# Kernel tuning notes

Hardware: AMD Instinct MI355X
Metric: run time of the kernel (lower is better)

The kernel has to match this reference:

```python
import jax, jax.numpy as jnp
import numpy as np

EPS = 1e-12  # torch F.normalize default eps
K, C = 64, 128  # num_clusters, dim


def _l2norm(v, axis):
    n = jnp.sqrt(jnp.sum(v * v, axis=axis, keepdims=True))
    return v / jnp.maximum(n, EPS)


def setup_inputs() -> dict:
    key = jax.random.key(0)
    k1, k2, k3, k4 = jax.random.split(key, 4)
    x = jax.random.normal(k1, (32, C, 64, 64), dtype=jnp.float32)
    centroids = jax.random.uniform(k2, (K, C), dtype=jnp.float32)
    # conv weight/bias initialized from centroids like _init_params (alpha=100)
    alpha = 100.0
    conv_w = 2.0 * alpha * centroids                     # [K, C] (1x1 conv)
    conv_b = -alpha * jnp.linalg.norm(centroids, axis=1) # [K]
    return {"x": x, "conv_w": conv_w, "conv_b": conv_b, "centroids": centroids}


def reference(x, conv_w, conv_b, centroids):
    N = x.shape[0]
    # descriptor-wise L2 normalization over channel dim
    x = _l2norm(x, axis=1)
    xf = x.reshape(N, C, -1)  # [N, C, P]
    # 1x1 conv == per-location linear: [N, K, P]
    logits = jnp.einsum('kc,ncp->nkp', conv_w, xf) + conv_b[None, :, None]
    soft_assign = jax.nn.softmax(logits, axis=1)  # softmax over clusters
    # vlad[n,k,c] = sum_p a[n,k,p] * (x[n,c,p] - centroids[k,c])
    # algebraic rewrite avoids the O(N*K*C*P) intermediate (same math)
    vlad = jnp.einsum('nkp,ncp->nkc', soft_assign, xf) \
        - soft_assign.sum(axis=2)[:, :, None] * centroids[None]
    vlad = _l2norm(vlad, axis=2)            # intra-normalization over C
    vlad = vlad.reshape(N, -1)              # [N, K*C]
    vlad = _l2norm(vlad, axis=1)            # global L2 norm
    return vlad
```

## Files before the change

kernel.cpp:

```cpp
#include <hip/hip_runtime.h>

typedef __attribute__((ext_vector_type(2))) float f2;
typedef __attribute__((ext_vector_type(4))) float f4;
typedef __attribute__((ext_vector_type(4))) float f32x4;
typedef __attribute__((ext_vector_type(4))) unsigned u32x4;
typedef __attribute__((ext_vector_type(8))) short bf16x8;

#define NK 64
#define NC 128
#define NP 4096
#define NN 32
#define EPSV 1e-12f

#define PCH 64
#define CPB 4
#define NGRPX (NP / (PCH * CPB))

#define WS_WF_SL 0
#define WS_SS    8192
#define WS_VP    (8192 + 32768)
#define WS_SLAB_TOTAL (WS_VP + NGRPX * NN * NK * NC)

#define FB_VLAD 0
#define FB_S    (NN * NK * NC)
#define FB_G    (FB_S + NN * NK)
#define FB_WF   (FB_G + NN)
#define FB_TOTAL (FB_WF + 8192)

__device__ __forceinline__ unsigned short f2bf(float x) {
  unsigned u = __builtin_bit_cast(unsigned, x);
  u += 0x7fffu + ((u >> 16) & 1u);
  return (unsigned short)(u >> 16);
}
__device__ __forceinline__ float bf2f(unsigned short h) {
  unsigned u = ((unsigned)h) << 16;
  return __builtin_bit_cast(float, u);
}
__device__ __forceinline__ unsigned cvtpk(float a, float b) {
  unsigned r;
  asm volatile("v_cvt_pk_bf16_f32 %0, %1, %2" : "=v"(r) : "v"(a), "v"(b));
  return r;
}
__device__ __forceinline__ float asf(unsigned u) { return __builtin_bit_cast(float, u); }

__device__ __forceinline__ void barrier_lds() {
  asm volatile("s_waitcnt lgkmcnt(0)" ::: "memory");
  __builtin_amdgcn_s_barrier();
  asm volatile("" ::: "memory");
  __builtin_amdgcn_sched_barrier(0);
}

__global__ void nv_zero(float* __restrict__ ws) {
  int i = blockIdx.x * blockDim.x + threadIdx.x;
  int stride = gridDim.x * blockDim.x;
  for (; i < FB_WF; i += stride) ws[i] = 0.0f;
}

__global__ void nv_wfrag(const float* __restrict__ conv_w, unsigned short* __restrict__ wfrag) {
  int idx = blockIdx.x * 256 + threadIdx.x;
  if (idx >= 2048) return;
  int lane = idx & 63, hl = (idx >> 6) & 1, ct = (idx >> 7) & 3, kt = idx >> 9;
  int r = lane & 15, g = lane >> 4;
  const float* src = conv_w + (16 * kt + r) * NC + 32 * ct + 8 * g;
  unsigned short o[8];
#pragma unroll
  for (int j = 0; j < 8; ++j) {
    float v = src[j];
    unsigned short h = f2bf(v);
    o[j] = hl ? f2bf(v - bf2f(h)) : h;
  }
  u32x4 pk;
#pragma unroll
  for (int m = 0; m < 4; ++m) pk[m] = (unsigned)o[2 * m] | ((unsigned)o[2 * m + 1] << 16);
  *reinterpret_cast<u32x4*>(wfrag + (size_t)idx * 8) = pk;
}

template <bool SLAB>
__global__ __launch_bounds__(512, 2)
void nv_main(const float* __restrict__ x, const unsigned short* __restrict__ wfrag,
             const float* __restrict__ conv_b, float* __restrict__ vout,
             float* __restrict__ sout) {
  __shared__ __align__(16) unsigned xhl_t[PCH][132];
  __shared__ __align__(16) unsigned short xh[NC][72];
  __shared__ __align__(16) unsigned short a_lds[NK][72];
  __shared__ __align__(16) unsigned short wf_lds[1024][8];
  __shared__ __align__(16) float mx_buf[2][PCH];
  __shared__ __align__(16) float sum_buf[2][PCH];

  const int tid = threadIdx.x;
  const int lane = tid & 63;
  const int w = tid >> 6;
  const int r = lane & 15;
  const int g = lane >> 4;
  const int n = blockIdx.y;
  const int p0loc = (w & 3) << 4;
  const int kp = w >> 2;
  const int ktg0 = kp << 1;
  const int kw = w & 3;
  const int ph = w >> 2;

  for (int s = tid; s < 1024; s += 512) {
    int gs = ((s >> 6) * 2) * 64 + (s & 63);
    *reinterpret_cast<u32x4*>(&wf_lds[s][0]) =
        *reinterpret_cast<const u32x4*>(wfrag + (size_t)gs * 8);
  }
  bf16x8 wlo_r[2][4];
#pragma unroll
  for (int kt2 = 0; kt2 < 2; ++kt2)
#pragma unroll
    for (int ct = 0; ct < 4; ++ct)
      wlo_r[kt2][ct] = *reinterpret_cast<const bf16x8*>(
          wfrag + ((size_t)(((ktg0 + kt2) * 4 + ct) * 2 + 1) * 64 + lane) * 8);
  float bb[2];
#pragma unroll
  for (int kt2 = 0; kt2 < 2; ++kt2) bb[kt2] = conv_b[16 * (ktg0 + kt2) + r];

  f32x4 vacc[8];
#pragma unroll
  for (int t = 0; t < 8; ++t) vacc[t] = (f32x4){0.f, 0.f, 0.f, 0.f};
  float s_part[2] = {0.f, 0.f};

  const int cst = tid & 127;
  const int pq = tid >> 7;
  const int swst = ((cst >> 3) & 3) << 3;
  const int pbase = blockIdx.x * (CPB * PCH);
  const float* xrow = x + ((size_t)n * NC + cst) * NP + 16 * pq;

  f4 pre[4];
  auto STAGE = [&]() {
#pragma unroll
    for (int q4 = 0; q4 < 4; ++q4) {
      f4 v = pre[q4];
      const int pl = 16 * pq + 4 * q4;
      unsigned h01 = cvtpk(v[0], v[1]);
      unsigned h23 = cvtpk(v[2], v[3]);
      float r0 = v[0] - asf(h01 << 16);
      float r1 = v[1] - asf(h01 & 0xffff0000u);
      float r2 = v[2] - asf(h23 << 16);
      float r3 = v[3] - asf(h23 & 0xffff0000u);
      unsigned l01 = cvtpk(r0, r1);
      unsigned l23 = cvtpk(r2, r3);
      const int pp = pl ^ swst;
      *reinterpret_cast<unsigned*>(&xh[cst][pp]) = h01;
      *reinterpret_cast<unsigned*>(&xh[cst][pp + 2]) = h23;
      xhl_t[pl + 0][cst] = __builtin_amdgcn_perm(h01, l01, 0x05040100u);
      xhl_t[pl + 1][cst] = __builtin_amdgcn_perm(h01, l01, 0x07060302u);
      xhl_t[pl + 2][cst] = __builtin_amdgcn_perm(h23, l23, 0x05040100u);
      xhl_t[pl + 3][cst] = __builtin_amdgcn_perm(h23, l23, 0x07060302u);
    }
  };

#pragma unroll
  for (int q4 = 0; q4 < 4; ++q4)
    pre[q4] = *reinterpret_cast<const f4*>(xrow + pbase + 4 * q4);
  STAGE();
  barrier_lds();

  for (int cc = 0; cc < CPB; ++cc) {
    if (cc + 1 < CPB) {
      const float* xb = xrow + pbase + (cc + 1) * PCH;
#pragma unroll
      for (int q4 = 0; q4 < 4; ++q4)
        pre[q4] = *reinterpret_cast<const f4*>(xb + 4 * q4);
    }
    f32x4 d1 = {0.f, 0.f, 0.f, 0.f}, d2 = {0.f, 0.f, 0.f, 0.f};
    f32x4 lac[2];
    lac[0] = (f32x4){0.f, 0.f, 0.f, 0.f};
    lac[1] = (f32x4){0.f, 0.f, 0.f, 0.f};
    __builtin_amdgcn_s_setprio(1);
#pragma unroll
    for (int ct = 0; ct < 4; ++ct) {
      const unsigned* row = &xhl_t[p0loc + r][32 * ct + 8 * g];
      u32x4 wA = *reinterpret_cast<const u32x4*>(row);
      u32x4 wB = *reinterpret_cast<const u32x4*>(row + 4);
      unsigned wv8[8] = {wA[0], wA[1], wA[2], wA[3], wB[0], wB[1], wB[2], wB[3]};
      u32x4 hh, ll;
#pragma unroll
      for (int m = 0; m < 4; ++m) {
        hh[m] = __builtin_amdgcn_perm(wv8[2 * m + 1], wv8[2 * m], 0x07060302u);
        ll[m] = __builtin_amdgcn_perm(wv8[2 * m + 1], wv8[2 * m], 0x05040100u);
      }
      bf16x8 Ah = __builtin_bit_cast(bf16x8, hh);
      bf16x8 Al = __builtin_bit_cast(bf16x8, ll);
      d1 = __builtin_amdgcn_mfma_f32_16x16x32_bf16(Ah, Ah, d1, 0, 0, 0);
      d2 = __builtin_amdgcn_mfma_f32_16x16x32_bf16(Ah, Al, d2, 0, 0, 0);
#pragma unroll
      for (int kt2 = 0; kt2 < 2; ++kt2) {
        const int kt4ct = (ktg0 + kt2) * 4 + ct;
        bf16x8 whi = *reinterpret_cast<const bf16x8*>(&wf_lds[kt4ct * 64 + lane][0]);
        lac[kt2] = __builtin_amdgcn_mfma_f32_16x16x32_bf16(Ah, whi, lac[kt2], 0, 0, 0);
        lac[kt2] = __builtin_amdgcn_mfma_f32_16x16x32_bf16(Al, whi, lac[kt2], 0, 0, 0);
        lac[kt2] = __builtin_amdgcn_mfma_f32_16x16x32_bf16(Ah, wlo_r[kt2][ct], lac[kt2], 0, 0, 0);
      }
    }
    __builtin_amdgcn_s_setprio(0);
    float nsq = d1[r & 3] + 2.0f * d2[r & 3];
    float ivv[4];
#pragma unroll
    for (int i = 0; i < 4; ++i) {
      float ns = __shfl(nsq, 20 * g + i);
      ivv[i] = 1.0f / fmaxf(sqrtf(ns), EPSV);
    }
    float lt[2][4], e[2][4], mpart[4], sp[4];
#pragma unroll
    for (int kt2 = 0; kt2 < 2; ++kt2)
#pragma unroll
      for (int i = 0; i < 4; ++i) lt[kt2][i] = lac[kt2][i] * ivv[i] + bb[kt2];
#pragma unroll
    for (int i = 0; i < 4; ++i) mpart[i] = fmaxf(lt[0][i], lt[1][i]);
#pragma unroll
    for (int o = 1; o <= 8; o <<= 1)
#pragma unroll
      for (int i = 0; i < 4; ++i) mpart[i] = fmaxf(mpart[i], __shfl_xor(mpart[i], o));
#pragma unroll
    for (int i = 0; i < 4; ++i) sp[i] = 0.f;
#pragma unroll
    for (int kt2 = 0; kt2 < 2; ++kt2)
#pragma unroll
      for (int i = 0; i < 4; ++i) {
        e[kt2][i] = __expf(lt[kt2][i] - mpart[i]);
        sp[i] += e[kt2][i];
      }
#pragma unroll
    for (int o = 1; o <= 8; o <<= 1)
#pragma unroll
      for (int i = 0; i < 4; ++i) sp[i] += __shfl_xor(sp[i], o);
    if (r < 4) mx_buf[kp][p0loc + 4 * g + r] = mpart[r];
    else if (r < 8) sum_buf[kp][p0loc + 4 * g + (r - 4)] = sp[r - 4];
    bf16x8 bx[8];
#pragma unroll
    for (int tcl = 0; tcl < 8; ++tcl) {
      const int c = (tcl << 4) + r;
      const int pblk = ((ph << 2) + g) ^ ((c >> 3) & 3);
      bx[tcl] = *reinterpret_cast<const bf16x8*>(&xh[c][pblk << 3]);
    }
    barrier_lds();
    {
      f4 m0 = *reinterpret_cast<const f4*>(&mx_buf[0][p0loc + 4 * g]);
      f4 m1 = *reinterpret_cast<const f4*>(&mx_buf[1][p0loc + 4 * g]);
      f4 s0 = *reinterpret_cast<const f4*>(&sum_buf[0][p0loc + 4 * g]);
      f4 s1 = *reinterpret_cast<const f4*>(&sum_buf[1][p0loc + 4 * g]);
      float fcorr[4];
#pragma unroll
      for (int i = 0; i < 4; ++i) {
        float m = fmaxf(m0[i], m1[i]);
        float c0 = __expf(m0[i] - m);
        float c1 = __expf(m1[i] - m);
        float tot = s0[i] * c0 + s1[i] * c1;
        fcorr[i] = (kp == 0 ? c0 : c1) / tot;
      }
#pragma unroll
      for (int kt2 = 0; kt2 < 2; ++kt2) {
        float av[4];
#pragma unroll
        for (int i = 0; i < 4; ++i) {
          float a = e[kt2][i] * fcorr[i];
          s_part[kt2] += a;
          av[i] = a * ivv[i];
        }
        unsigned* arow = reinterpret_cast<unsigned*>(&a_lds[16 * (ktg0 + kt2) + r][p0loc + 4 * g]);
        arow[0] = cvtpk(av[0], av[1]);
        arow[1] = cvtpk(av[2], av[3]);
      }
    }
    barrier_lds();
    {
      bf16x8 af = *reinterpret_cast<const bf16x8*>(&a_lds[16 * kw + r][32 * ph + 8 * g]);
      __builtin_amdgcn_s_setprio(1);
#pragma unroll
      for (int tcl = 0; tcl < 8; ++tcl)
        vacc[tcl] = __builtin_amdgcn_mfma_f32_16x16x32_bf16(af, bx[tcl], vacc[tcl], 0, 0, 0);
      __builtin_amdgcn_s_setprio(0);
    }
    if (cc + 1 < CPB) {
      STAGE();
      barrier_lds();
    }
  }

  float* cbuf = reinterpret_cast<float*>(&xhl_t[0][0]);
  float* s_red = cbuf + 8192;
  if (w < 4) {
#pragma unroll
    for (int tcl = 0; tcl < 8; ++tcl)
#pragma unroll
      for (int i = 0; i < 4; ++i)
        cbuf[kw * 2048 + (4 * g + i) * 128 + (tcl << 4) + r] = vacc[tcl][i];
  }
#pragma unroll
  for (int kt2 = 0; kt2 < 2; ++kt2) {
    float v = s_part[kt2];
    v += __shfl_xor(v, 16);
    v += __shfl_xor(v, 32);
    if (g == 0) s_red[(kp * 4 + (w & 3)) * 32 + kt2 * 16 + r] = v;
  }
  barrier_lds();
  if (w >= 4) {
#pragma unroll
    for (int tcl = 0; tcl < 8; ++tcl)
#pragma unroll
      for (int i = 0; i < 4; ++i) {
        const int idx = kw * 2048 + (4 * g + i) * 128 + (tcl << 4) + r;
        float v = vacc[tcl][i] + cbuf[idx];
        if constexpr (SLAB) cbuf[idx] = v;
        else atomicAdd(&vout[((size_t)n * NK + 16 * kw + 4 * g + i) * NC + (tcl << 4) + r], v);
      }
  }
  if (tid < 64) {
    float S = 0.f;
#pragma unroll
    for (int pt = 0; pt < 4; ++pt) S += s_red[((tid >> 5) * 4 + pt) * 32 + (tid & 31)];
    if constexpr (SLAB) sout[((size_t)blockIdx.x * NN + n) * NK + tid] = S;
    else atomicAdd(&sout[n * NK + tid], S);
  }
  if constexpr (SLAB) {
    barrier_lds();
    float* dst = vout + ((size_t)blockIdx.x * NN + n) * (NK * NC);
#pragma unroll
    for (int m = 0; m < 4; ++m) {
      const int idx = m * 512 + tid;
      *reinterpret_cast<f4*>(dst + 4 * idx) = *reinterpret_cast<const f4*>(cbuf + 4 * idx);
    }
  }
}

__global__ __launch_bounds__(256)
void nv_finalize2(const float* __restrict__ vin, const float* __restrict__ sin,
                  const float* __restrict__ centroids, float* __restrict__ out) {
  const int wv = threadIdx.x >> 6;
  const int lane = threadIdx.x & 63;
  const int k = blockIdx.x * 4 + wv;
  const int n = blockIdx.y;
  const int c0 = lane * 2;
  f2 v = {0.f, 0.f};
#pragma unroll
  for (int sx = 0; sx < NGRPX; ++sx) {
    const float* vr = vin + ((size_t)sx * NN + n) * (NK * NC) + k * NC;
    f2 t = *reinterpret_cast<const f2*>(vr + c0);
    v.x += t.x;
    v.y += t.y;
  }
  float sv = (lane < 16) ? sin[((size_t)lane * NN + n) * NK + k] : 0.f;
#pragma unroll
  for (int o = 1; o <= 8; o <<= 1) sv += __shfl_xor(sv, o);
  float S = __shfl(sv, 0);
  f2 ce = *reinterpret_cast<const f2*>(centroids + k * NC + c0);
  v.x -= S * ce.x;
  v.y -= S * ce.y;
  float ss = v.x * v.x + v.y * v.y;
#pragma unroll
  for (int o = 1; o < 64; o <<= 1) ss += __shfl_xor(ss, o);
  float inv = 0.125f / fmaxf(sqrtf(ss), EPSV);
  f2 ov = {v.x * inv, v.y * inv};
  *reinterpret_cast<f2*>(out + ((size_t)n * NK + k) * NC + c0) = ov;
}

__global__ void nv_finalize(const float* __restrict__ vin, const float* __restrict__ sin,
                            const float* __restrict__ centroids,
                            float* __restrict__ out, float* __restrict__ gnorm) {
  const int k = blockIdx.x;
  const int n = blockIdx.y;
  const int t = threadIdx.x;
  float S = sin[n * NK + k];
  const size_t base = ((size_t)n * NK + k) * NC;
  float v0 = vin[base + t] - S * centroids[k * NC + t];
  float v1 = vin[base + t + 64] - S * centroids[k * NC + t + 64];
  float ss = v0 * v0 + v1 * v1;
#pragma unroll
  for (int off = 1; off < 64; off <<= 1) ss += __shfl_xor(ss, off);
  float inv = 1.0f / fmaxf(sqrtf(ss), EPSV);
  out[base + t] = v0 * inv;
  out[base + t + 64] = v1 * inv;
  if (t == 0) atomicAdd(&gnorm[n], ss * inv * inv);
}

__global__ void nv_scale(float* __restrict__ out, const float* __restrict__ gnorm) {
  int i = blockIdx.x * blockDim.x + threadIdx.x;
  int n = i >> 13;
  out[i] *= 1.0f / fmaxf(sqrtf(gnorm[n]), EPSV);
}

extern "C" void kernel_launch(void* const* d_in, const int* in_sizes, int n_in,
                              void* d_out, int out_size, void* d_ws, size_t ws_size,
                              hipStream_t stream) {
  const float* x = (const float*)d_in[0];
  const float* conv_w = (const float*)d_in[1];
  const float* conv_b = (const float*)d_in[2];
  const float* centroids = (const float*)d_in[3];
  float* out = (float*)d_out;
  float* ws = (float*)d_ws;

  if (ws_size >= (size_t)WS_SLAB_TOTAL * sizeof(float)) {
    unsigned short* wfrag = (unsigned short*)(ws + WS_WF_SL);
    float* sp = ws + WS_SS;
    float* vp = ws + WS_VP;
    nv_wfrag<<<8, 256, 0, stream>>>(conv_w, wfrag);
    nv_main<true><<<dim3(NGRPX, NN), 512, 0, stream>>>(x, wfrag, conv_b, vp, sp);
    nv_finalize2<<<dim3(NK / 4, NN), 256, 0, stream>>>(vp, sp, centroids, out);
  } else {
    float* vlad_acc = ws + FB_VLAD;
    float* s_acc = ws + FB_S;
    float* gnorm = ws + FB_G;
    unsigned short* wfrag = (unsigned short*)(ws + FB_WF);
    nv_zero<<<256, 256, 0, stream>>>(ws);
    nv_wfrag<<<8, 256, 0, stream>>>(conv_w, wfrag);
    nv_main<false><<<dim3(NGRPX, NN), 512, 0, stream>>>(x, wfrag, conv_b, vlad_acc, s_acc);
    nv_finalize<<<dim3(NK, NN), 64, 0, stream>>>(vlad_acc, s_acc, centroids, out, gnorm);
    nv_scale<<<1024, 256, 0, stream>>>(out, gnorm);
  }
}
```

Measured before the change: 50.77 us.

## Fuse weight bf16 split into main kernel and restructure per-chunk staging loop

Removes the separate nv_wfrag launch. Each block of the main kernel now converts conv_w to hi/lo bf16 fragments itself while the first x chunk loads. The chunk loop is also reorganised so staging happens at the top of each iteration, followed by a barrier. The xh B-fragments for the vlad MFMA are read from LDS right before use instead of being prefetched before the softmax barriers, and the s_setprio hints are dropped. This saves one kernel launch and the workspace round trip, but every block now redoes the weight conversion and one extra barrier is added per chunk.

```diff
diff --git a/kernel.cpp b/kernel.cpp
--- a/kernel.cpp
+++ b/kernel.cpp
@@ -16,16 +16,14 @@
 #define CPB 4
 #define NGRPX (NP / (PCH * CPB))
 
-#define WS_WF_SL 0
-#define WS_SS    8192
-#define WS_VP    (8192 + 32768)
+#define WS_SS    0
+#define WS_VP    32768
 #define WS_SLAB_TOTAL (WS_VP + NGRPX * NN * NK * NC)
 
 #define FB_VLAD 0
 #define FB_S    (NN * NK * NC)
 #define FB_G    (FB_S + NN * NK)
-#define FB_WF   (FB_G + NN)
-#define FB_TOTAL (FB_WF + 8192)
+#define FB_TOTAL (FB_G + NN)
 
 __device__ __forceinline__ unsigned short f2bf(float x) {
   unsigned u = __builtin_bit_cast(unsigned, x);
@@ -53,31 +51,12 @@
 __global__ void nv_zero(float* __restrict__ ws) {
   int i = blockIdx.x * blockDim.x + threadIdx.x;
   int stride = gridDim.x * blockDim.x;
-  for (; i < FB_WF; i += stride) ws[i] = 0.0f;
-}
-
-__global__ void nv_wfrag(const float* __restrict__ conv_w, unsigned short* __restrict__ wfrag) {
-  int idx = blockIdx.x * 256 + threadIdx.x;
-  if (idx >= 2048) return;
-  int lane = idx & 63, hl = (idx >> 6) & 1, ct = (idx >> 7) & 3, kt = idx >> 9;
-  int r = lane & 15, g = lane >> 4;
-  const float* src = conv_w + (16 * kt + r) * NC + 32 * ct + 8 * g;
-  unsigned short o[8];
-#pragma unroll
-  for (int j = 0; j < 8; ++j) {
-    float v = src[j];
-    unsigned short h = f2bf(v);
-    o[j] = hl ? f2bf(v - bf2f(h)) : h;
-  }
-  u32x4 pk;
-#pragma unroll
-  for (int m = 0; m < 4; ++m) pk[m] = (unsigned)o[2 * m] | ((unsigned)o[2 * m + 1] << 16);
-  *reinterpret_cast<u32x4*>(wfrag + (size_t)idx * 8) = pk;
+  for (; i < FB_TOTAL; i += stride) ws[i] = 0.0f;
 }
 
 template <bool SLAB>
 __global__ __launch_bounds__(512, 2)
-void nv_main(const float* __restrict__ x, const unsigned short* __restrict__ wfrag,
+void nv_main(const float* __restrict__ x, const float* __restrict__ conv_w,
              const float* __restrict__ conv_b, float* __restrict__ vout,
              float* __restrict__ sout) {
   __shared__ __align__(16) unsigned xhl_t[PCH][132];
@@ -99,27 +78,6 @@
   const int kw = w & 3;
   const int ph = w >> 2;
 
-  for (int s = tid; s < 1024; s += 512) {
-    int gs = ((s >> 6) * 2) * 64 + (s & 63);
-    *reinterpret_cast<u32x4*>(&wf_lds[s][0]) =
-        *reinterpret_cast<const u32x4*>(wfrag + (size_t)gs * 8);
-  }
-  bf16x8 wlo_r[2][4];
-#pragma unroll
-  for (int kt2 = 0; kt2 < 2; ++kt2)
-#pragma unroll
-    for (int ct = 0; ct < 4; ++ct)
-      wlo_r[kt2][ct] = *reinterpret_cast<const bf16x8*>(
-          wfrag + ((size_t)(((ktg0 + kt2) * 4 + ct) * 2 + 1) * 64 + lane) * 8);
-  float bb[2];
-#pragma unroll
-  for (int kt2 = 0; kt2 < 2; ++kt2) bb[kt2] = conv_b[16 * (ktg0 + kt2) + r];
-
-  f32x4 vacc[8];
-#pragma unroll
-  for (int t = 0; t < 8; ++t) vacc[t] = (f32x4){0.f, 0.f, 0.f, 0.f};
-  float s_part[2] = {0.f, 0.f};
-
   const int cst = tid & 127;
   const int pq = tid >> 7;
   const int swst = ((cst >> 3) & 3) << 3;
@@ -127,7 +85,55 @@
   const float* xrow = x + ((size_t)n * NC + cst) * NP + 16 * pq;
 
   f4 pre[4];
-  auto STAGE = [&]() {
+#pragma unroll
+  for (int q4 = 0; q4 < 4; ++q4)
+    pre[q4] = *reinterpret_cast<const f4*>(xrow + pbase + 4 * q4);
+
+#pragma unroll
+  for (int sI = 0; sI < 2; ++sI) {
+    const int s = tid + sI * 512;
+    const int kt4 = s >> 6;
+    const int ls = s & 63;
+    const int rs = ls & 15, gs = ls >> 4;
+    const float* src = conv_w + (16 * (kt4 >> 2) + rs) * NC + 32 * (kt4 & 3) + 8 * gs;
+    f4 va = *reinterpret_cast<const f4*>(src);
+    f4 vb = *reinterpret_cast<const f4*>(src + 4);
+    u32x4 pk;
+    pk[0] = cvtpk(va[0], va[1]);
+    pk[1] = cvtpk(va[2], va[3]);
+    pk[2] = cvtpk(vb[0], vb[1]);
+    pk[3] = cvtpk(vb[2], vb[3]);
+    *reinterpret_cast<u32x4*>(&wf_lds[s][0]) = pk;
+  }
+  bf16x8 wlo_r[2][4];
+#pragma unroll
+  for (int kt2 = 0; kt2 < 2; ++kt2)
+#pragma unroll
+    for (int ct = 0; ct < 4; ++ct) {
+      const float* src = conv_w + (16 * (ktg0 + kt2) + r) * NC + 32 * ct + 8 * g;
+      f4 va = *reinterpret_cast<const f4*>(src);
+      f4 vb = *reinterpret_cast<const f4*>(src + 4);
+      unsigned h01 = cvtpk(va[0], va[1]);
+      unsigned h23 = cvtpk(va[2], va[3]);
+      unsigned h45 = cvtpk(vb[0], vb[1]);
+      unsigned h67 = cvtpk(vb[2], vb[3]);
+      u32x4 lo;
+      lo[0] = cvtpk(va[0] - asf(h01 << 16), va[1] - asf(h01 & 0xffff0000u));
+      lo[1] = cvtpk(va[2] - asf(h23 << 16), va[3] - asf(h23 & 0xffff0000u));
+      lo[2] = cvtpk(vb[0] - asf(h45 << 16), vb[1] - asf(h45 & 0xffff0000u));
+      lo[3] = cvtpk(vb[2] - asf(h67 << 16), vb[3] - asf(h67 & 0xffff0000u));
+      wlo_r[kt2][ct] = __builtin_bit_cast(bf16x8, lo);
+    }
+  float bb[2];
+#pragma unroll
+  for (int kt2 = 0; kt2 < 2; ++kt2) bb[kt2] = conv_b[16 * (ktg0 + kt2) + r];
+
+  f32x4 vacc[8];
+#pragma unroll
+  for (int t = 0; t < 8; ++t) vacc[t] = (f32x4){0.f, 0.f, 0.f, 0.f};
+  float s_part[2] = {0.f, 0.f};
+
+  for (int cc = 0; cc < CPB; ++cc) {
 #pragma unroll
     for (int q4 = 0; q4 < 4; ++q4) {
       f4 v = pre[q4];
@@ -148,15 +154,7 @@
       xhl_t[pl + 2][cst] = __builtin_amdgcn_perm(h23, l23, 0x05040100u);
       xhl_t[pl + 3][cst] = __builtin_amdgcn_perm(h23, l23, 0x07060302u);
     }
-  };
-
-#pragma unroll
-  for (int q4 = 0; q4 < 4; ++q4)
-    pre[q4] = *reinterpret_cast<const f4*>(xrow + pbase + 4 * q4);
-  STAGE();
-  barrier_lds();
-
-  for (int cc = 0; cc < CPB; ++cc) {
+    barrier_lds();
     if (cc + 1 < CPB) {
       const float* xb = xrow + pbase + (cc + 1) * PCH;
 #pragma unroll
@@ -167,7 +165,6 @@
     f32x4 lac[2];
     lac[0] = (f32x4){0.f, 0.f, 0.f, 0.f};
     lac[1] = (f32x4){0.f, 0.f, 0.f, 0.f};
-    __builtin_amdgcn_s_setprio(1);
 #pragma unroll
     for (int ct = 0; ct < 4; ++ct) {
       const unsigned* row = &xhl_t[p0loc + r][32 * ct + 8 * g];
@@ -193,7 +190,6 @@
         lac[kt2] = __builtin_amdgcn_mfma_f32_16x16x32_bf16(Ah, wlo_r[kt2][ct], lac[kt2], 0, 0, 0);
       }
     }
-    __builtin_amdgcn_s_setprio(0);
     float nsq = d1[r & 3] + 2.0f * d2[r & 3];
     float ivv[4];
 #pragma unroll
@@ -227,13 +223,6 @@
       for (int i = 0; i < 4; ++i) sp[i] += __shfl_xor(sp[i], o);
     if (r < 4) mx_buf[kp][p0loc + 4 * g + r] = mpart[r];
     else if (r < 8) sum_buf[kp][p0loc + 4 * g + (r - 4)] = sp[r - 4];
-    bf16x8 bx[8];
-#pragma unroll
-    for (int tcl = 0; tcl < 8; ++tcl) {
-      const int c = (tcl << 4) + r;
-      const int pblk = ((ph << 2) + g) ^ ((c >> 3) & 3);
-      bx[tcl] = *reinterpret_cast<const bf16x8*>(&xh[c][pblk << 3]);
-    }
     barrier_lds();
     {
       f4 m0 = *reinterpret_cast<const f4*>(&mx_buf[0][p0loc + 4 * g]);
@@ -266,16 +255,15 @@
     barrier_lds();
     {
       bf16x8 af = *reinterpret_cast<const bf16x8*>(&a_lds[16 * kw + r][32 * ph + 8 * g]);
-      __builtin_amdgcn_s_setprio(1);
-#pragma unroll
-      for (int tcl = 0; tcl < 8; ++tcl)
-        vacc[tcl] = __builtin_amdgcn_mfma_f32_16x16x32_bf16(af, bx[tcl], vacc[tcl], 0, 0, 0);
-      __builtin_amdgcn_s_setprio(0);
-    }
-    if (cc + 1 < CPB) {
-      STAGE();
-      barrier_lds();
-    }
+#pragma unroll
+      for (int tcl = 0; tcl < 8; ++tcl) {
+        const int c = (tcl << 4) + r;
+        const int pblk = ((ph << 2) + g) ^ ((c >> 3) & 3);
+        bf16x8 bx = *reinterpret_cast<const bf16x8*>(&xh[c][pblk << 3]);
+        vacc[tcl] = __builtin_amdgcn_mfma_f32_16x16x32_bf16(af, bx, vacc[tcl], 0, 0, 0);
+      }
+    }
+    barrier_lds();
   }
 
   float* cbuf = reinterpret_cast<float*>(&xhl_t[0][0]);
@@ -391,20 +379,16 @@
   float* ws = (float*)d_ws;
 
   if (ws_size >= (size_t)WS_SLAB_TOTAL * sizeof(float)) {
-    unsigned short* wfrag = (unsigned short*)(ws + WS_WF_SL);
     float* sp = ws + WS_SS;
     float* vp = ws + WS_VP;
-    nv_wfrag<<<8, 256, 0, stream>>>(conv_w, wfrag);
-    nv_main<true><<<dim3(NGRPX, NN), 512, 0, stream>>>(x, wfrag, conv_b, vp, sp);
+    nv_main<true><<<dim3(NGRPX, NN), 512, 0, stream>>>(x, conv_w, conv_b, vp, sp);
     nv_finalize2<<<dim3(NK / 4, NN), 256, 0, stream>>>(vp, sp, centroids, out);
   } else {
     float* vlad_acc = ws + FB_VLAD;
     float* s_acc = ws + FB_S;
     float* gnorm = ws + FB_G;
-    unsigned short* wfrag = (unsigned short*)(ws + FB_WF);
     nv_zero<<<256, 256, 0, stream>>>(ws);
-    nv_wfrag<<<8, 256, 0, stream>>>(conv_w, wfrag);
-    nv_main<false><<<dim3(NGRPX, NN), 512, 0, stream>>>(x, wfrag, conv_b, vlad_acc, s_acc);
+    nv_main<false><<<dim3(NGRPX, NN), 512, 0, stream>>>(x, conv_w, conv_b, vlad_acc, s_acc);
     nv_finalize<<<dim3(NK, NN), 64, 0, stream>>>(vlad_acc, s_acc, centroids, out, gnorm);
     nv_scale<<<1024, 256, 0, stream>>>(out, gnorm);
   }
```

New measurement: 51.77 us. Within noise of the previous version (+2.0%).

## Restructure chunk loop: stage at top, LDS norm broadcast, load x fragments lazily

Applied to the files above, without the earlier changes.

Moves the bf16 staging of x into the top of the per-chunk loop, followed by a barrier. A barrier is now added at the end of every iteration, after the vlad MFMAs. The inverse-norm broadcast switches from four cross-lane shuffles to one LDS write and read per point. The B fragments of x are loaded right before each MFMA instead of being hoisted before the softmax barriers, which lowers register pressure but exposes LDS latency. The s_setprio hints are removed. This adds one extra barrier per chunk, and the prefetched global load now has less compute to hide behind.

```diff
diff --git a/kernel.cpp b/kernel.cpp
--- a/kernel.cpp
+++ b/kernel.cpp
@@ -84,6 +84,7 @@
   __shared__ __align__(16) unsigned short xh[NC][72];
   __shared__ __align__(16) unsigned short a_lds[NK][72];
   __shared__ __align__(16) unsigned short wf_lds[1024][8];
+  __shared__ __align__(16) float inv_lds[PCH];
   __shared__ __align__(16) float mx_buf[2][PCH];
   __shared__ __align__(16) float sum_buf[2][PCH];
 
@@ -127,7 +128,11 @@
   const float* xrow = x + ((size_t)n * NC + cst) * NP + 16 * pq;
 
   f4 pre[4];
-  auto STAGE = [&]() {
+#pragma unroll
+  for (int q4 = 0; q4 < 4; ++q4)
+    pre[q4] = *reinterpret_cast<const f4*>(xrow + pbase + 4 * q4);
+
+  for (int cc = 0; cc < CPB; ++cc) {
 #pragma unroll
     for (int q4 = 0; q4 < 4; ++q4) {
       f4 v = pre[q4];
@@ -148,15 +153,7 @@
       xhl_t[pl + 2][cst] = __builtin_amdgcn_perm(h23, l23, 0x05040100u);
       xhl_t[pl + 3][cst] = __builtin_amdgcn_perm(h23, l23, 0x07060302u);
     }
-  };
-
-#pragma unroll
-  for (int q4 = 0; q4 < 4; ++q4)
-    pre[q4] = *reinterpret_cast<const f4*>(xrow + pbase + 4 * q4);
-  STAGE();
-  barrier_lds();
-
-  for (int cc = 0; cc < CPB; ++cc) {
+    barrier_lds();
     if (cc + 1 < CPB) {
       const float* xb = xrow + pbase + (cc + 1) * PCH;
 #pragma unroll
@@ -167,7 +164,6 @@
     f32x4 lac[2];
     lac[0] = (f32x4){0.f, 0.f, 0.f, 0.f};
     lac[1] = (f32x4){0.f, 0.f, 0.f, 0.f};
-    __builtin_amdgcn_s_setprio(1);
 #pragma unroll
     for (int ct = 0; ct < 4; ++ct) {
       const unsigned* row = &xhl_t[p0loc + r][32 * ct + 8 * g];
@@ -193,14 +189,14 @@
         lac[kt2] = __builtin_amdgcn_mfma_f32_16x16x32_bf16(Ah, wlo_r[kt2][ct], lac[kt2], 0, 0, 0);
       }
     }
-    __builtin_amdgcn_s_setprio(0);
-    float nsq = d1[r & 3] + 2.0f * d2[r & 3];
-    float ivv[4];
-#pragma unroll
-    for (int i = 0; i < 4; ++i) {
-      float ns = __shfl(nsq, 20 * g + i);
-      ivv[i] = 1.0f / fmaxf(sqrtf(ns), EPSV);
-    }
+    if ((r >> 2) == g) {
+      int i = r & 3;
+      float nsq = d1[i] + 2.0f * d2[i];
+      inv_lds[p0loc + r] = 1.0f / fmaxf(sqrtf(nsq), EPSV);
+    }
+    asm volatile("s_waitcnt lgkmcnt(0)" ::: "memory");
+    __builtin_amdgcn_sched_barrier(0);
+    f4 ivv = *reinterpret_cast<const f4*>(&inv_lds[p0loc + 4 * g]);
     float lt[2][4], e[2][4], mpart[4], sp[4];
 #pragma unroll
     for (int kt2 = 0; kt2 < 2; ++kt2)
@@ -227,13 +223,6 @@
       for (int i = 0; i < 4; ++i) sp[i] += __shfl_xor(sp[i], o);
     if (r < 4) mx_buf[kp][p0loc + 4 * g + r] = mpart[r];
     else if (r < 8) sum_buf[kp][p0loc + 4 * g + (r - 4)] = sp[r - 4];
-    bf16x8 bx[8];
-#pragma unroll
-    for (int tcl = 0; tcl < 8; ++tcl) {
-      const int c = (tcl << 4) + r;
-      const int pblk = ((ph << 2) + g) ^ ((c >> 3) & 3);
-      bx[tcl] = *reinterpret_cast<const bf16x8*>(&xh[c][pblk << 3]);
-    }
     barrier_lds();
     {
       f4 m0 = *reinterpret_cast<const f4*>(&mx_buf[0][p0loc + 4 * g]);
@@ -266,16 +255,15 @@
     barrier_lds();
     {
       bf16x8 af = *reinterpret_cast<const bf16x8*>(&a_lds[16 * kw + r][32 * ph + 8 * g]);
-      __builtin_amdgcn_s_setprio(1);
-#pragma unroll
-      for (int tcl = 0; tcl < 8; ++tcl)
-        vacc[tcl] = __builtin_amdgcn_mfma_f32_16x16x32_bf16(af, bx[tcl], vacc[tcl], 0, 0, 0);
-      __builtin_amdgcn_s_setprio(0);
-    }
-    if (cc + 1 < CPB) {
-      STAGE();
-      barrier_lds();
-    }
+#pragma unroll
+      for (int tcl = 0; tcl < 8; ++tcl) {
+        const int c = (tcl << 4) + r;
+        const int pblk = ((ph << 2) + g) ^ ((c >> 3) & 3);
+        bf16x8 bx = *reinterpret_cast<const bf16x8*>(&xh[c][pblk << 3]);
+        vacc[tcl] = __builtin_amdgcn_mfma_f32_16x16x32_bf16(af, bx, vacc[tcl], 0, 0, 0);
+      }
+    }
+    barrier_lds();
   }
 
   float* cbuf = reinterpret_cast<float*>(&xhl_t[0][0]);
```

Result: faster. 47.64 us (-6.2%).
